# Optimization experiments

Measured on AMD Instinct MI355X. Metric: run time of the kernel, lower is better.

## Reference

```python
import jax, jax.numpy as jnp
from jax import lax
import numpy as np

T, N, C, S = 256, 64, 7356, 32
NEG = -1e9  # finite stand-in for -inf (keeps grads clean)


def setup_inputs() -> dict:
    key = jax.random.key(0)
    k1, k2, k3 = jax.random.split(key, 3)
    out = jax.random.normal(k1, (T, N, C), dtype=jnp.float32)
    # PyTorch CTCLoss expects log-probs; the module passes `out` through as-is,
    # so we feed log_softmax'd activations (what the surrounding model produces).
    out = jax.nn.log_softmax(out, axis=-1)
    text = jax.random.randint(k2, (N, S), 1, C)            # labels in [1, C-1], blank=0 excluded
    pre_len = jnp.full((N,), T, dtype=jnp.int64 if jax.config.jax_enable_x64 else jnp.int32)
    lengths = jax.random.randint(k3, (N,), 16, S + 1)       # target lengths in [16, 32]
    return {"out": out, "text": text, "pre_len": pre_len, "lengths": lengths}


def _ctc_loss_mean(logp, targets, input_lengths, target_lengths):
    # logp: [T, N, C] log-probs; targets: [N, S]; lengths: [N]
    Tt, Nn, _ = logp.shape
    Ss = targets.shape[1]
    L = 2 * Ss + 1
    # Extended label sequence: blank, l1, blank, l2, ..., blank
    ext = jnp.zeros((Nn, L), dtype=targets.dtype).at[:, 1::2].set(targets)  # [N, L]
    ext_m2 = jnp.concatenate([jnp.zeros((Nn, 2), dtype=ext.dtype), ext[:, :-2]], axis=1)
    skip = (jnp.arange(L)[None, :] >= 2) & (ext != 0) & (ext != ext_m2)      # [N, L]

    # Gather per-frame log-probs of extended labels: [T, N, L]
    lp_ext = logp[:, jnp.arange(Nn)[:, None], ext]

    alpha0 = jnp.full((Nn, L), NEG, dtype=logp.dtype)
    alpha0 = alpha0.at[:, 0].set(lp_ext[0, :, 0]).at[:, 1].set(lp_ext[0, :, 1])

    negcol1 = jnp.full((Nn, 1), NEG, dtype=logp.dtype)
    negcol2 = jnp.full((Nn, 2), NEG, dtype=logp.dtype)

    def step(alpha, lp_t):
        s1 = jnp.concatenate([negcol1, alpha[:, :-1]], axis=1)
        s2 = jnp.concatenate([negcol2, alpha[:, :-2]], axis=1)
        a = jnp.logaddexp(alpha, s1)
        a = jnp.logaddexp(a, jnp.where(skip, s2, NEG))
        new = a + lp_t
        return new, new

    _, alphas_rest = lax.scan(step, alpha0, lp_ext[1:])
    alphas = jnp.concatenate([alpha0[None], alphas_rest], axis=0)  # [T, N, L]

    n_idx = jnp.arange(Nn)
    a_end = alphas[input_lengths - 1, n_idx]                        # [N, L]
    l_last = 2 * target_lengths                                     # index of final blank
    log_like = jnp.logaddexp(a_end[n_idx, l_last], a_end[n_idx, l_last - 1])
    # reduction='mean': per-sample loss / target_length, then mean over batch
    per = -log_like / target_lengths.astype(logp.dtype)
    return jnp.mean(per)


def reference(out, text, pre_len, lengths):
    loss = _ctc_loss_mean(out, text, pre_len, lengths)
    weight = jnp.square(1.0 - jnp.exp(-loss))
    return weight * loss
```

## Files before the change

kernel.cpp:

```cpp
#include <hip/hip_runtime.h>

#define Tt 256
#define Nn 64
#define Cc 7356
#define Ss 32
#define NEGf (-1.0e9f)
#define LOG2E 1.4426950408889634f
#define LN2   0.6931471805599453f

#define WS_CNT   0
#define WS_PAIR  1
#define WS_SLOTS 65
#define WS_VEC   130
#define WS_NEED_BYTES ((130 + Nn * 130) * 4)

__device__ __forceinline__ float fexp2(float x) { return __builtin_amdgcn_exp2f(x); }
__device__ __forceinline__ float flog2(float x) { return __builtin_amdgcn_logf(x); }

__device__ __forceinline__ float dpp_shr1(float x, float fallback) {
    int r = __builtin_amdgcn_update_dpp(__float_as_int(fallback), __float_as_int(x),
                                        0x138 , 0xf, 0xf, false);
    return __int_as_float(r);
}
__device__ __forceinline__ float dpp_shl1(float x, float fallback) {
    int r = __builtin_amdgcn_update_dpp(__float_as_int(fallback), __float_as_int(x),
                                        0x130 , 0xf, 0xf, false);
    return __int_as_float(r);
}
__device__ __forceinline__ float bcast(float x, int l) {
    return __int_as_float(__builtin_amdgcn_readlane(__float_as_int(x), l));
}
__device__ __forceinline__ float lse2(float a, float b) {
    float m = fmaxf(a, b);
    return m + flog2(fexp2(a - m) + fexp2(b - m));
}

__global__ __launch_bounds__(256) void ctc_half_kernel(
    const float* __restrict__ logp, const int* __restrict__ text,
    const int* __restrict__ lengths, float* __restrict__ ws,
    float* __restrict__ out)
{
    __shared__ float lp2[128][64];

    const int tid  = threadIdx.x;
    const int lane = tid & 63;
    const int wid  = tid >> 6;
    const int n    = blockIdx.x & (Nn - 1);
    const bool bwd = blockIdx.x >= Nn;
    const size_t tstr = (size_t)Nn * Cc;

    int ch = (lane & 1) ? 0 : text[n * Ss + (lane >> 1)];

    {
        const int t0 = (bwd ? 128 : 0) + wid * 32;
        const float* src = logp + (size_t)t0 * tstr + (size_t)n * Cc + ch;
        float v[32];
        #pragma unroll
        for (int i = 0; i < 32; ++i) v[i] = src[(size_t)i * tstr];
        #pragma unroll
        for (int i = 0; i < 32; ++i) lp2[wid * 32 + i][lane] = v[i] * LOG2E;
    }
    __syncthreads();
    if (wid != 0) return;

    const int len = lengths[n];
    float* vec = ws + WS_VEC + n * 130 + (bwd ? 65 : 0);
    float stv, st0, lpb[16];

    if (!bwd) {
        int ch_m2 = __shfl_up(ch, 2, 64);
        const bool skipd = (lane >= 2) && !(lane & 1) && (ch != ch_m2);

#define FWD_STEP(LP) { \
        float lp = (LP); \
        float lpblank = bcast(lp, 1); \
        float s1 = dpp_shr1(stv, st0); \
        float s2 = dpp_shr1(s1, NEGf); \
        float s2m = skipd ? s2 : NEGf; \
        float m  = fmaxf(fmaxf(stv, s1), s2m); \
        float e  = fexp2(stv - m) + fexp2(s1 - m) + fexp2(s2m - m); \
        stv = (m + lp) + flog2(e); \
        st0 = st0 + lpblank; }

        #pragma unroll
        for (int i = 0; i < 16; ++i) lpb[i] = lp2[i][lane];
        stv = (lane == 0) ? lpb[0] : NEGf;
        st0 = bcast(lpb[0], 1);
        #pragma unroll
        for (int j = 1; j < 16; ++j) FWD_STEP(lpb[j]);
        for (int c = 1; c < 8; ++c) {
            #pragma unroll
            for (int i = 0; i < 16; ++i) lpb[i] = lp2[16 * c + i][lane];
            #pragma unroll
            for (int j = 0; j < 16; ++j) FWD_STEP(lpb[j]);
        }
#undef FWD_STEP
        float s1 = dpp_shr1(stv, st0);
        float s2 = dpp_shr1(s1, NEGf);
        float s2m = skipd ? s2 : NEGf;
        float m  = fmaxf(fmaxf(stv, s1), s2m);
        float e  = fexp2(stv - m) + fexp2(s1 - m) + fexp2(s2m - m);
        vec[1 + lane] = m + flog2(e);
        if (lane == 0) vec[0] = st0;
    } else {
        int ch_p2 = __shfl_down(ch, 2, 64);
        const bool skips = !(lane & 1) && (lane <= 61) && (ch != ch_p2);

#define BWD_STEP(LP) { \
        float lp = (LP); \
        float lpblank = bcast(lp, 1); \
        float b1 = bcast(stv, 0); \
        float u1 = dpp_shl1(stv, NEGf); \
        float u2 = dpp_shl1(u1, NEGf); \
        float u2m = skips ? u2 : NEGf; \
        float m  = fmaxf(fmaxf(stv, u1), u2m); \
        float e  = fexp2(stv - m) + fexp2(u1 - m) + fexp2(u2m - m); \
        float nb = (m + lp) + flog2(e); \
        float m2 = fmaxf(st0, b1); \
        st0 = (m2 + lpblank) + flog2(fexp2(st0 - m2) + fexp2(b1 - m2)); \
        stv = nb; }

        #pragma unroll
        for (int i = 0; i < 16; ++i) lpb[i] = lp2[127 - i][lane];
        int llast = 2 * len;
        stv = (lane == llast - 2 || lane == llast - 1) ? lpb[0] : NEGf;
        st0 = NEGf;
        #pragma unroll
        for (int j = 1; j < 16; ++j) BWD_STEP(lpb[j]);
        for (int c = 1; c < 8; ++c) {
            #pragma unroll
            for (int i = 0; i < 16; ++i) lpb[i] = lp2[127 - 16 * c - i][lane];
            #pragma unroll
            for (int j = 0; j < 16; ++j) BWD_STEP(lpb[j]);
        }
#undef BWD_STEP
        vec[1 + lane] = stv;
        if (lane == 0) vec[0] = st0;
    }

    __threadfence();
    int* pair = (int*)ws + WS_PAIR;
    int old = -1;
    if (lane == 0)
        old = __hip_atomic_fetch_add(&pair[n], 1, __ATOMIC_ACQ_REL, __HIP_MEMORY_SCOPE_AGENT);
    old = __shfl(old, 0, 64);
    if (old == 0) return;

    const float* va = ws + WS_VEC + n * 130;
    const float* vb = va + 65;
    float local = __hip_atomic_load(&va[lane], __ATOMIC_ACQUIRE, __HIP_MEMORY_SCOPE_AGENT)
                + __hip_atomic_load(&vb[lane], __ATOMIC_ACQUIRE, __HIP_MEMORY_SCOPE_AGENT);
    if (lane == 0) {
        float a64 = __hip_atomic_load(&va[64], __ATOMIC_ACQUIRE, __HIP_MEMORY_SCOPE_AGENT)
                  + __hip_atomic_load(&vb[64], __ATOMIC_ACQUIRE, __HIP_MEMORY_SCOPE_AGENT);
        local = lse2(local, a64);
    }
    #pragma unroll
    for (int off = 1; off < 64; off <<= 1)
        local = lse2(local, __shfl_xor(local, off, 64));
    float per = -(local * LN2) / (float)len;

    float* slots = ws + WS_SLOTS;
    int* counter = (int*)ws + WS_CNT;
    old = -1;
    if (lane == 0) {
        __hip_atomic_store(&slots[n], per, __ATOMIC_RELEASE, __HIP_MEMORY_SCOPE_AGENT);
        __threadfence();
        old = __hip_atomic_fetch_add(counter, 1, __ATOMIC_ACQ_REL, __HIP_MEMORY_SCOPE_AGENT);
    }
    old = __shfl(old, 0, 64);
    if (old == Nn - 1) {
        __threadfence();
        float v = __hip_atomic_load(&slots[lane], __ATOMIC_ACQUIRE, __HIP_MEMORY_SCOPE_AGENT);
        #pragma unroll
        for (int off = 32; off > 0; off >>= 1)
            v += __shfl_down(v, off, 64);
        if (lane == 0) {
            float loss = v * (1.0f / (float)Nn);
            float w = 1.0f - __expf(-loss);
            out[0] = w * w * loss;
        }
    }
}

#define PFD 16
__global__ __launch_bounds__(64) void ctc_alpha_kernel(
    const float* __restrict__ logp, const int* __restrict__ text,
    const int* __restrict__ pre_len, const int* __restrict__ lengths,
    float* __restrict__ per_out)
{
    const int n = blockIdx.x; const int lane = threadIdx.x;
    int ch = 0;
    if (lane & 1) ch = text[n * Ss + (lane >> 1)];
    int ch_m2 = __shfl_up(ch, 2, 64);
    bool skip = (lane >= 2) && (ch != 0) && (ch != ch_m2);
    const size_t rowbase = (size_t)n * Cc, tstride = (size_t)Nn * Cc;
    float lp0 = logp[rowbase + ch] * LOG2E;
    float alpha = (lane < 2) ? lp0 : NEGf, alpha64 = NEGf;
    const int stop_t = pre_len[n] - 1;
    float sv = alpha, sv64 = alpha64;
    float lpb[PFD];
    #pragma unroll
    for (int i = 0; i < PFD; ++i)
        lpb[i] = logp[(size_t)(1 + i) * tstride + rowbase + ch] * LOG2E;
#define CTC_STEP(LPREG) { \
        float lp = (LPREG); float lpblank = bcast(lp, 0); float a63 = bcast(alpha, 63); \
        float s1 = dpp_shr1(alpha, NEGf); float s2 = dpp_shr1(s1, NEGf); \
        float s2m = skip ? s2 : NEGf; \
        float m = fmaxf(fmaxf(alpha, s1), s2m); \
        float e = fexp2(alpha - m) + fexp2(s1 - m) + fexp2(s2m - m); \
        float na = (m + lp) + flog2(e); \
        float m2 = fmaxf(alpha64, a63); \
        alpha64 = (m2 + lpblank) + flog2(fexp2(alpha64 - m2) + fexp2(a63 - m2)); \
        alpha = na; if (t == stop_t) { sv = alpha; sv64 = alpha64; } ++t; }
    int t = 1;
    for (int blk = 0; blk < 15; ++blk) {
        #pragma unroll
        for (int j = 0; j < PFD; ++j) {
            float lpj = lpb[j]; int tpf = t + PFD;
            if (tpf < Tt) lpb[j] = logp[(size_t)tpf * tstride + rowbase + ch] * LOG2E;
            CTC_STEP(lpj);
        }
    }
    #pragma unroll
    for (int j = 0; j < PFD - 1; ++j) { CTC_STEP(lpb[j]); }
#undef CTC_STEP
    int len = lengths[n]; int l_last = 2 * len;
    float v1 = __shfl(sv, l_last < 64 ? l_last : 63, 64);
    if (l_last == 64) v1 = sv64;
    float v2 = __shfl(sv, l_last - 1, 64);
    float per = -(lse2(v1, v2) * LN2) / (float)len;
    if (lane == 0) per_out[n] = per;
}

__global__ __launch_bounds__(64) void finalize_kernel(
    const float* __restrict__ per, float* __restrict__ out)
{
    int lane = threadIdx.x;
    float v = per[lane];
    #pragma unroll
    for (int off = 32; off > 0; off >>= 1) v += __shfl_down(v, off, 64);
    if (lane == 0) {
        float loss = v * (1.0f / (float)Nn);
        float w = 1.0f - __expf(-loss);
        out[0] = w * w * loss;
    }
}

extern "C" void kernel_launch(void* const* d_in, const int* in_sizes, int n_in,
                              void* d_out, int out_size, void* d_ws, size_t ws_size,
                              hipStream_t stream) {
    const float* logp    = (const float*)d_in[0];
    const int*   text    = (const int*)d_in[1];
    const int*   pre_len = (const int*)d_in[2];
    const int*   lengths = (const int*)d_in[3];

    if (ws_size >= (size_t)WS_NEED_BYTES) {
        hipMemsetAsync(d_ws, 0, 65 * sizeof(int), stream);
        ctc_half_kernel<<<2 * Nn, 256, 0, stream>>>(logp, text, lengths,
                                                    (float*)d_ws, (float*)d_out);
    } else {
        float* per = (float*)d_ws;
        ctc_alpha_kernel<<<Nn, 64, 0, stream>>>(logp, text, pre_len, lengths, per);
        finalize_kernel<<<1, 64, 0, stream>>>(per, (float*)d_out);
    }
}
```

Baseline: 37.59 us.

## Split gather across partner blocks and overlap middle-frame loads with recursion

Each forward and backward half now gathers only its first 64 frames into shared memory and starts the recursion. Partner blocks gather the remaining 64 frames per half into a compact workspace buffer and signal readiness through flags. The recursion waves spin on those flags, then read the staged frames, with a direct-global fallback if the flag never arrives. This aims to hide the strided gather latency behind the sequential recursion, at the cost of a larger workspace, an extra memset, and spin-waiting that depends on partner blocks being co-resident.

After: 51.13 us. 36.0% more time.

```diff
diff --git a/kernel.cpp b/kernel.cpp
--- a/kernel.cpp
+++ b/kernel.cpp
@@ -11,8 +11,10 @@
 #define WS_CNT   0
 #define WS_PAIR  1
 #define WS_SLOTS 65
-#define WS_VEC   130
-#define WS_NEED_BYTES ((130 + Nn * 130) * 4)
+#define WS_FLAG  129
+#define WS_VEC   260
+#define WS_CMP   8704
+#define WS_NEED_BYTES ((WS_CMP + 128 * Nn * 64) * 4)
 
 __device__ __forceinline__ float fexp2(float x) { return __builtin_amdgcn_exp2f(x); }
 __device__ __forceinline__ float flog2(float x) { return __builtin_amdgcn_logf(x); }
@@ -35,39 +37,68 @@
     return m + flog2(fexp2(a - m) + fexp2(b - m));
 }
 
-__global__ __launch_bounds__(256) void ctc_half_kernel(
+__global__ __launch_bounds__(256) void ctc_split_kernel(
     const float* __restrict__ logp, const int* __restrict__ text,
     const int* __restrict__ lengths, float* __restrict__ ws,
     float* __restrict__ out)
 {
-    __shared__ float lp2[128][64];
+    __shared__ float lp2[64][64];
 
     const int tid  = threadIdx.x;
     const int lane = tid & 63;
     const int wid  = tid >> 6;
-    const int n    = blockIdx.x & (Nn - 1);
-    const bool bwd = blockIdx.x >= Nn;
+    const bool partner = blockIdx.x >= 128;
+    const int sub  = partner ? blockIdx.x - 128 : blockIdx.x;
+    const int n    = sub & (Nn - 1);
+    const int h    = sub >> 6;
     const size_t tstr = (size_t)Nn * Cc;
 
     int ch = (lane & 1) ? 0 : text[n * Ss + (lane >> 1)];
+    const float* lb = logp + (size_t)n * Cc + ch;
+    float* cmp = ws + WS_CMP;
+    int* flags = (int*)ws + WS_FLAG;
+
+    if (partner) {
+        const int r0 = wid * 16;
+        float v[16];
+        #pragma unroll
+        for (int i = 0; i < 16; ++i) {
+            int t = (h == 0 ? 64 : 128) + r0 + i;
+            v[i] = lb[(size_t)t * tstr];
+        }
+        #pragma unroll
+        for (int i = 0; i < 16; ++i) {
+            int t = (h == 0 ? 64 : 128) + r0 + i;
+            cmp[(size_t)(t - 64) * (Nn * 64) + n * 64 + lane] = v[i] * LOG2E;
+        }
+        __threadfence();
+        __syncthreads();
+        if (tid == 0)
+            __hip_atomic_store(&flags[h * 64 + n], 1,
+                               __ATOMIC_RELEASE, __HIP_MEMORY_SCOPE_AGENT);
+        return;
+    }
 
     {
-        const int t0 = (bwd ? 128 : 0) + wid * 32;
-        const float* src = logp + (size_t)t0 * tstr + (size_t)n * Cc + ch;
-        float v[32];
-        #pragma unroll
-        for (int i = 0; i < 32; ++i) v[i] = src[(size_t)i * tstr];
-        #pragma unroll
-        for (int i = 0; i < 32; ++i) lp2[wid * 32 + i][lane] = v[i] * LOG2E;
+        float v[16];
+        #pragma unroll
+        for (int i = 0; i < 16; ++i) {
+            int o = wid * 16 + i;
+            int t = (h == 0) ? o : 255 - o;
+            v[i] = lb[(size_t)t * tstr];
+        }
+        #pragma unroll
+        for (int i = 0; i < 16; ++i)
+            lp2[wid * 16 + i][lane] = v[i] * LOG2E;
     }
     __syncthreads();
     if (wid != 0) return;
 
     const int len = lengths[n];
-    float* vec = ws + WS_VEC + n * 130 + (bwd ? 65 : 0);
+    float* vec = ws + WS_VEC + n * 130 + h * 65;
     float stv, st0, lpb[16];
 
-    if (!bwd) {
+    if (h == 0) {
         int ch_m2 = __shfl_up(ch, 2, 64);
         const bool skipd = (lane >= 2) && !(lane & 1) && (ch != ch_m2);
 
@@ -88,13 +119,39 @@
         st0 = bcast(lpb[0], 1);
         #pragma unroll
         for (int j = 1; j < 16; ++j) FWD_STEP(lpb[j]);
-        for (int c = 1; c < 8; ++c) {
+        for (int c = 1; c < 4; ++c) {
             #pragma unroll
             for (int i = 0; i < 16; ++i) lpb[i] = lp2[16 * c + i][lane];
             #pragma unroll
             for (int j = 0; j < 16; ++j) FWD_STEP(lpb[j]);
         }
+        int* fp = &flags[0 * 64 + n];
+        bool ok = false;
+        for (int it = 0; it < 131072; ++it) {
+            if (__hip_atomic_load(fp, __ATOMIC_RELAXED, __HIP_MEMORY_SCOPE_AGENT)) { ok = true; break; }
+            __builtin_amdgcn_s_sleep(2);
+        }
+        if (ok) {
+            (void)__hip_atomic_load(fp, __ATOMIC_ACQUIRE, __HIP_MEMORY_SCOPE_AGENT);
+            const float* cb = cmp + n * 64 + lane;
+            for (int c = 0; c < 4; ++c) {
+                #pragma unroll
+                for (int i = 0; i < 16; ++i)
+                    lpb[i] = cb[(size_t)(16 * c + i) * (Nn * 64)];
+                #pragma unroll
+                for (int j = 0; j < 16; ++j) FWD_STEP(lpb[j]);
+            }
+        } else {
+            for (int c = 0; c < 4; ++c) {
+                #pragma unroll
+                for (int i = 0; i < 16; ++i)
+                    lpb[i] = lb[(size_t)(64 + 16 * c + i) * tstr] * LOG2E;
+                #pragma unroll
+                for (int j = 0; j < 16; ++j) FWD_STEP(lpb[j]);
+            }
+        }
 #undef FWD_STEP
+        int ch_m2b = __shfl_up(ch, 2, 64); (void)ch_m2b;
         float s1 = dpp_shr1(stv, st0);
         float s2 = dpp_shr1(s1, NEGf);
         float s2m = skipd ? s2 : NEGf;
@@ -121,17 +178,42 @@
         stv = nb; }
 
         #pragma unroll
-        for (int i = 0; i < 16; ++i) lpb[i] = lp2[127 - i][lane];
+        for (int i = 0; i < 16; ++i) lpb[i] = lp2[i][lane];
         int llast = 2 * len;
         stv = (lane == llast - 2 || lane == llast - 1) ? lpb[0] : NEGf;
         st0 = NEGf;
         #pragma unroll
         for (int j = 1; j < 16; ++j) BWD_STEP(lpb[j]);
-        for (int c = 1; c < 8; ++c) {
+        for (int c = 1; c < 4; ++c) {
             #pragma unroll
-            for (int i = 0; i < 16; ++i) lpb[i] = lp2[127 - 16 * c - i][lane];
+            for (int i = 0; i < 16; ++i) lpb[i] = lp2[16 * c + i][lane];
             #pragma unroll
             for (int j = 0; j < 16; ++j) BWD_STEP(lpb[j]);
+        }
+        int* fp = &flags[1 * 64 + n];
+        bool ok = false;
+        for (int it = 0; it < 131072; ++it) {
+            if (__hip_atomic_load(fp, __ATOMIC_RELAXED, __HIP_MEMORY_SCOPE_AGENT)) { ok = true; break; }
+            __builtin_amdgcn_s_sleep(2);
+        }
+        if (ok) {
+            (void)__hip_atomic_load(fp, __ATOMIC_ACQUIRE, __HIP_MEMORY_SCOPE_AGENT);
+            const float* cb = cmp + n * 64 + lane;
+            for (int c = 0; c < 4; ++c) {
+                #pragma unroll
+                for (int i = 0; i < 16; ++i)
+                    lpb[i] = cb[(size_t)(191 - 16 * c - i - 64) * (Nn * 64)];
+                #pragma unroll
+                for (int j = 0; j < 16; ++j) BWD_STEP(lpb[j]);
+            }
+        } else {
+            for (int c = 0; c < 4; ++c) {
+                #pragma unroll
+                for (int i = 0; i < 16; ++i)
+                    lpb[i] = lb[(size_t)(191 - 16 * c - i) * tstr] * LOG2E;
+                #pragma unroll
+                for (int j = 0; j < 16; ++j) BWD_STEP(lpb[j]);
+            }
         }
 #undef BWD_STEP
         vec[1 + lane] = stv;
@@ -256,9 +338,9 @@
     const int*   lengths = (const int*)d_in[3];
 
     if (ws_size >= (size_t)WS_NEED_BYTES) {
-        hipMemsetAsync(d_ws, 0, 65 * sizeof(int), stream);
-        ctc_half_kernel<<<2 * Nn, 256, 0, stream>>>(logp, text, lengths,
-                                                    (float*)d_ws, (float*)d_out);
+        hipMemsetAsync(d_ws, 0, WS_VEC * sizeof(int), stream);
+        ctc_split_kernel<<<256, 256, 0, stream>>>(logp, text, lengths,
+                                                  (float*)d_ws, (float*)d_out);
     } else {
         float* per = (float*)d_ws;
         ctc_alpha_kernel<<<Nn, 64, 0, stream>>>(logp, text, pre_len, lengths, per);
```
